# Kernel optimization log

Hardware: AMD Instinct MI355X
Metric: run time of the kernel (lower is better)

## Reference

```python
import jax, jax.numpy as jnp
import numpy as np

B, S, DM, H, DK, DH = 8, 1024, 512, 8, 32, 64
LN_EPS = 1e-5
NEG_SLOPE = 0.01  # torch LeakyReLU default


def _l2norm(t, axis=-1, eps=1e-12):
    # matches F.normalize(p=2): x / max(||x||, eps)
    n = jnp.sqrt(jnp.sum(t * t, axis=axis, keepdims=True))
    return t / jnp.maximum(n, eps)


def _layernorm(t, w, b, eps=LN_EPS):
    mu = jnp.mean(t, axis=-1, keepdims=True)
    var = jnp.mean((t - mu) ** 2, axis=-1, keepdims=True)
    return (t - mu) * jax.lax.rsqrt(var + eps) * w + b


def setup_inputs() -> dict:
    key = jax.random.key(0)
    ks = jax.random.split(key, 16)
    x = jax.random.normal(ks[0], (B, S, DM), dtype=jnp.float32)
    # causal-style mask: True = masked (upper triangle)
    attn_mask = jnp.broadcast_to(jnp.triu(jnp.ones((S, S), dtype=bool), k=1), (B, S, S))
    pairwise_dist = jax.random.uniform(ks[1], (B, S, S), dtype=jnp.float32)
    s = 0.02
    return {
        "x": x,
        "attn_mask": attn_mask,
        "pairwise_dist": pairwise_dist,
        "Wq": jax.random.normal(ks[2], (H, DK, DM), dtype=jnp.float32) * s,
        "Wk": jax.random.normal(ks[3], (H, DK, DM), dtype=jnp.float32) * s,
        "Wv": jax.random.normal(ks[4], (H, DH, DM), dtype=jnp.float32) * s,
        "omega": jnp.ones((H,), dtype=jnp.float32),
        "Wo": jax.random.normal(ks[5], (DM, H * DH), dtype=jnp.float32) * s,
        "bo": jnp.zeros((DM,), dtype=jnp.float32),
        "Wf": jax.random.normal(ks[6], (DM, DM), dtype=jnp.float32) * s,
        "bf": jnp.zeros((DM,), dtype=jnp.float32),
        "ln1_w": jnp.ones((DM,), dtype=jnp.float32),
        "ln1_b": jnp.zeros((DM,), dtype=jnp.float32),
        "ln2_w": jnp.ones((DM,), dtype=jnp.float32),
        "ln2_b": jnp.zeros((DM,), dtype=jnp.float32),
    }


def _encoder_layer(x, attn_mask, pairwise_dist, Wq, Wk, Wv, omega,
                   Wo, bo, Wf, bf, ln1_w, ln1_b, ln2_w, ln2_b):
    # --- multi-head self-attention, all heads batched ---
    q = _l2norm(jnp.einsum('bsd,hkd->hbsk', x, Wq))   # [H,B,S,DK]
    k = _l2norm(jnp.einsum('bsd,hkd->hbsk', x, Wk))
    v = jnp.einsum('bsd,hvd->hbsv', x, Wv)            # [H,B,S,DH]
    scores = jnp.einsum('hbsk,hbtk->hbst', q, k)      # cosine-sim, [H,B,S,S]
    # distance bias: exp(-omega*d) - 1, detached in the original
    r = jax.lax.stop_gradient(
        jnp.exp(-omega[:, None, None, None] * pairwise_dist[None]) - 1.0)
    scores = scores + r
    scores = jnp.where(attn_mask[None], -jnp.inf, scores)
    # custom softmax: exp(x) / (sum + 1); exp(-inf)=0 handles masking
    z = jnp.exp(scores)
    attn = z / (jnp.sum(z, axis=-1, keepdims=True) + 1.0)
    y = jnp.einsum('hbst,hbtv->hbsv', attn, v)        # [H,B,S,DH]
    y = jnp.transpose(y, (1, 2, 0, 3)).reshape(x.shape[0], x.shape[1], -1)  # concat heads
    x_attn = y @ Wo.T + bo
    # --- residual + LN + FFN (dropout p=0 -> identity) ---
    z1 = _layernorm(x + x_attn, ln1_w, ln1_b)
    z_ff = jax.nn.leaky_relu(z1 @ Wf.T + bf, negative_slope=NEG_SLOPE)
    return _layernorm(z1 + z_ff, ln2_w, ln2_b)


def reference(x, attn_mask, pairwise_dist, Wq, Wk, Wv, omega,
              Wo, bo, Wf, bf, ln1_w, ln1_b, ln2_w, ln2_b):
    return _encoder_layer(x, attn_mask, pairwise_dist, Wq, Wk, Wv, omega,
                          Wo, bo, Wf, bf, ln1_w, ln1_b, ln2_w, ln2_b)
```

## Files before the change

### kernel.cpp

```cpp
#include <hip/hip_runtime.h>
#include <hip/hip_bf16.h>
#include <math.h>
#include <stdint.h>

#define BB 8
#define SS 1024
#define DMM 512
#define HH 8
#define DKK 32
#define DHH 64

typedef __bf16 bf16x8 __attribute__((ext_vector_type(8)));
typedef float f32x4 __attribute__((ext_vector_type(4)));

__device__ __forceinline__ void gll16(const void* g, void* l) {
  __builtin_amdgcn_global_load_lds(
      (const __attribute__((address_space(1))) void*)(uintptr_t)g,
      (__attribute__((address_space(3))) void*)(uint32_t)(uintptr_t)l,
      16, 0, 0);
}

__device__ __forceinline__ uint4 pack8(const float4 a, const float4 b) {
  union { __hip_bfloat162 h2[4]; uint4 u; } p;
  p.h2[0] = __float22bfloat162_rn(make_float2(a.x, a.y));
  p.h2[1] = __float22bfloat162_rn(make_float2(a.z, a.w));
  p.h2[2] = __float22bfloat162_rn(make_float2(b.x, b.y));
  p.h2[3] = __float22bfloat162_rn(make_float2(b.z, b.w));
  return p.u;
}

__global__ __launch_bounds__(256) void cvt_all(
    const float* __restrict__ x, const float* __restrict__ Wq,
    const float* __restrict__ Wk, const float* __restrict__ Wv,
    const float* __restrict__ Wo, const float* __restrict__ Wf,
    __bf16* __restrict__ xb, __bf16* __restrict__ Wcat,
    __bf16* __restrict__ Wob, __bf16* __restrict__ Wfb) {
  size_t i = ((size_t)blockIdx.x * 256 + threadIdx.x) * 8;
  const float* s;
  __bf16* d;
  size_t off;
  if (i < 4194304) { s = x; d = xb + i; off = i; }
  else {
    size_t j = i - 4194304;
    if (j < 524288) {
      d = Wcat + j;
      if (j < 131072) { s = Wq; off = j; }
      else if (j < 262144) { s = Wk; off = j - 131072; }
      else { s = Wv; off = j - 262144; }
    } else {
      size_t jj = j - 524288;
      if (jj < 262144) { s = Wo; d = Wob + jj; off = jj; }
      else { s = Wf; d = Wfb + (jj - 262144); off = jj - 262144; }
    }
  }
  float4 a = *(const float4*)&s[off];
  float4 b = *(const float4*)&s[off + 4];
  *(uint4*)d = pack8(a, b);
}

__global__ __launch_bounds__(256) void gemm_qkv(
    const __bf16* __restrict__ A, const __bf16* __restrict__ W,
    __bf16* __restrict__ Qg, __bf16* __restrict__ Kg,
    __bf16* __restrict__ Vrow) {
  __shared__ __bf16 As[128 * 32];
  __shared__ __bf16 Bs[128 * 32];
  const int tid = threadIdx.x;
  const int n0 = blockIdx.x * 128;
  const int m0 = blockIdx.y * 128;
  const int lane = tid & 63;
  const int w = tid >> 6;
  const int wm = (w & 1) * 64, wn = (w >> 1) * 64;
  const int fr = lane & 15, quad = lane >> 4;
  const int srow = lane >> 2;
  const int schunk = (lane & 3) ^ ((lane >> 3) & 3);

  f32x4 acc[4][4];
#pragma unroll
  for (int mi = 0; mi < 4; ++mi)
#pragma unroll
    for (int ni = 0; ni < 4; ++ni) acc[mi][ni] = (f32x4){0.f, 0.f, 0.f, 0.f};

  for (int kt = 0; kt < 512; kt += 32) {
    __syncthreads();
#pragma unroll
    for (int j = 0; j < 2; ++j) {
      const int seg = w * 2 + j;
      const int row = seg * 16 + srow;
      gll16(&A[(size_t)(m0 + row) * 512 + kt + schunk * 8], &As[seg * 512]);
      gll16(&W[(size_t)(n0 + row) * 512 + kt + schunk * 8], &Bs[seg * 512]);
    }
    __syncthreads();

    bf16x8 af[4], bf[4];
    const int rsw = (quad ^ ((fr >> 1) & 3)) * 8;
#pragma unroll
    for (int mi = 0; mi < 4; ++mi)
      af[mi] = *(const bf16x8*)&As[(wm + mi * 16 + fr) * 32 + rsw];
#pragma unroll
    for (int ni = 0; ni < 4; ++ni)
      bf[ni] = *(const bf16x8*)&Bs[(wn + ni * 16 + fr) * 32 + rsw];
#pragma unroll
    for (int mi = 0; mi < 4; ++mi)
#pragma unroll
      for (int ni = 0; ni < 4; ++ni)
        acc[mi][ni] = __builtin_amdgcn_mfma_f32_16x16x32_bf16(
            af[mi], bf[ni], acc[mi][ni], 0, 0, 0);
  }

  const int er = quad * 4;
  const int ec = fr;
  if (n0 < 512) {
    const bool isq = (n0 < 256);
    __bf16* G = isq ? Qg : Kg;
    const int nb = isq ? n0 : n0 - 256;
#pragma unroll
    for (int mi = 0; mi < 4; ++mi) {
#pragma unroll
      for (int p = 0; p < 2; ++p) {
        const int hh = (nb + wn + p * 32) >> 5;
#pragma unroll
        for (int r = 0; r < 4; ++r) {
          float v0 = acc[mi][2 * p][r], v1 = acc[mi][2 * p + 1][r];
          float ss = v0 * v0 + v1 * v1;
          ss += __shfl_xor(ss, 1, 64);
          ss += __shfl_xor(ss, 2, 64);
          ss += __shfl_xor(ss, 4, 64);
          ss += __shfl_xor(ss, 8, 64);
          const float sc = 1.0f / fmaxf(sqrtf(ss), 1e-12f);
          const int mm = m0 + wm + mi * 16 + er + r;
          const int bb = mm >> 10, s = mm & 1023;
          __bf16* gp = G + ((size_t)(bb * 8 + hh) * 1024 + s) * 32;
          gp[ec] = (__bf16)(v0 * sc);
          gp[16 + ec] = (__bf16)(v1 * sc);
        }
      }
    }
  } else {
#pragma unroll
    for (int mi = 0; mi < 4; ++mi)
#pragma unroll
      for (int ni = 0; ni < 4; ++ni) {
        const int n = n0 - 512 + wn + ni * 16 + ec;
#pragma unroll
        for (int r = 0; r < 4; ++r) {
          const int mm = m0 + wm + mi * 16 + er + r;
          Vrow[(size_t)mm * 512 + n] = (__bf16)acc[mi][ni][r];
        }
      }
  }
}

template <int MODE>
__global__ __launch_bounds__(256) void gemm_bf16(
    const __bf16* __restrict__ A, const __bf16* __restrict__ W,
    const float* __restrict__ bias, const float* __restrict__ resid,
    float* __restrict__ C, int N) {
  __shared__ __bf16 As[128 * 32];
  __shared__ __bf16 Bs[128 * 32];
  const int tid = threadIdx.x;
  const int n0 = blockIdx.x * 128;
  const int m0 = blockIdx.y * 128;
  const int lane = tid & 63;
  const int w = tid >> 6;
  const int wm = (w & 1) * 64, wn = (w >> 1) * 64;
  const int fr = lane & 15, quad = lane >> 4;
  const int srow = lane >> 2;
  const int schunk = (lane & 3) ^ ((lane >> 3) & 3);

  f32x4 acc[4][4];
#pragma unroll
  for (int mi = 0; mi < 4; ++mi)
#pragma unroll
    for (int ni = 0; ni < 4; ++ni) acc[mi][ni] = (f32x4){0.f, 0.f, 0.f, 0.f};

  for (int kt = 0; kt < 512; kt += 32) {
    __syncthreads();
#pragma unroll
    for (int j = 0; j < 2; ++j) {
      const int seg = w * 2 + j;
      const int row = seg * 16 + srow;
      gll16(&A[(size_t)(m0 + row) * 512 + kt + schunk * 8], &As[seg * 512]);
      gll16(&W[(size_t)(n0 + row) * 512 + kt + schunk * 8], &Bs[seg * 512]);
    }
    __syncthreads();

    bf16x8 af[4], bf[4];
    const int rsw = (quad ^ ((fr >> 1) & 3)) * 8;
#pragma unroll
    for (int mi = 0; mi < 4; ++mi)
      af[mi] = *(const bf16x8*)&As[(wm + mi * 16 + fr) * 32 + rsw];
#pragma unroll
    for (int ni = 0; ni < 4; ++ni)
      bf[ni] = *(const bf16x8*)&Bs[(wn + ni * 16 + fr) * 32 + rsw];
#pragma unroll
    for (int mi = 0; mi < 4; ++mi)
#pragma unroll
      for (int ni = 0; ni < 4; ++ni)
        acc[mi][ni] = __builtin_amdgcn_mfma_f32_16x16x32_bf16(
            af[mi], bf[ni], acc[mi][ni], 0, 0, 0);
  }

  const int er = quad * 4;
  const int ec = fr;
#pragma unroll
  for (int mi = 0; mi < 4; ++mi) {
#pragma unroll
    for (int ni = 0; ni < 4; ++ni) {
      const int n = n0 + wn + ni * 16 + ec;
      float bsv = bias[n];
#pragma unroll
      for (int r = 0; r < 4; ++r) {
        const int m = m0 + wm + mi * 16 + er + r;
        float v = acc[mi][ni][r];
        if (MODE == 1) {
          v += bsv + resid[(size_t)m * 512 + n];
        } else {
          float g = v + bsv;
          g = g > 0.f ? g : 0.01f * g;
          v = resid[(size_t)m * 512 + n] + g;
        }
        C[(size_t)m * N + n] = v;
      }
    }
  }
}

__global__ __launch_bounds__(256) void v_transpose(
    const __bf16* __restrict__ Vrow, __bf16* __restrict__ Vt) {
  __shared__ __bf16 vt[64][136];
  const int bh = blockIdx.x;
  const int b = bh >> 3, h = bh & 7;
  const int sb = blockIdx.y * 128;
  const int tid = threadIdx.x;
#pragma unroll
  for (int i = 0; i < 8; ++i) {
    int idx = tid + i * 256;
    int t = idx >> 4, vd4 = (idx & 15) * 4;
    union { uint2 u; __bf16 e[4]; } v;
    v.u = *(const uint2*)&Vrow[((size_t)(b * 1024 + sb + t)) * 512 + h * 64 + vd4];
    vt[vd4 + 0][t] = v.e[0];
    vt[vd4 + 1][t] = v.e[1];
    vt[vd4 + 2][t] = v.e[2];
    vt[vd4 + 3][t] = v.e[3];
  }
  __syncthreads();
  {
    const int vd = tid >> 2, tseg = (tid & 3) * 32;
    uint4* o = (uint4*)(Vt + (size_t)bh * 65536 + (size_t)vd * 1024 + sb + tseg);
#pragma unroll
    for (int j = 0; j < 4; ++j)
      o[j] = *(const uint4*)&vt[vd][tseg + j * 8];
  }
}

__global__ __launch_bounds__(256) void attn_fused(
    const __bf16* __restrict__ Qg, const __bf16* __restrict__ Kg,
    const __bf16* __restrict__ Vt, const float* __restrict__ dist,
    const float* __restrict__ omega, __bf16* __restrict__ y) {
  __shared__ __bf16 Ks[64 * 32];
  __shared__ __bf16 Vs[64 * 64];
  __shared__ __bf16 zbuf[4][16][72];

  const int b = blockIdx.x;
  const int s0 = (15 - blockIdx.y) * 64;
  const int h = blockIdx.z;
  const int bh = b * 8 + h;
  const int tid = threadIdx.x;
  const int lane = tid & 63;
  const int w = tid >> 6;
  const int q = lane >> 4;
  const int m = lane & 15;
  const float om = omega[h];

  const int sl = s0 + w * 16 + m;
  const bf16x8 bq = *(const bf16x8*)&Qg[((size_t)bh * 1024 + sl) * 32 + q * 8];
  const int kswz = (q ^ ((m >> 1) & 3)) * 8;

  f32x4 acc[4];
#pragma unroll
  for (int ni = 0; ni < 4; ++ni) acc[ni] = (f32x4){0.f, 0.f, 0.f, 0.f};
  float zsum = 0.0f;
  const int ntiles = (s0 >> 6) + 1;

  for (int tt = 0; tt < ntiles; ++tt) {
    const int t0 = tt * 64;
    __syncthreads();
    {
      int row = tid >> 2, p = tid & 3;
      uint4 v = *(const uint4*)&Kg[((size_t)bh * 1024 + t0 + row) * 32 + p * 8];
      *(uint4*)&Ks[row * 32 + ((p ^ ((row >> 1) & 3)) * 8)] = v;
    }
#pragma unroll
    for (int i = 0; i < 2; ++i) {
      int idx = tid + i * 256;
      int vd = idx >> 3, p = idx & 7;
      uint4 v = *(const uint4*)&Vt[(size_t)bh * 65536 + (size_t)vd * 1024 + t0 + p * 8];
      *(uint4*)&Vs[vd * 64 + ((p ^ (vd & 7)) * 8)] = v;
    }
    float4 dv[4];
#pragma unroll
    for (int mi = 0; mi < 4; ++mi)
      dv[mi] = *(const float4*)&dist[((size_t)b * 1024 + sl) * 1024 + t0 + 16 * mi + q * 4];
    __syncthreads();

#pragma unroll
    for (int mi = 0; mi < 4; ++mi) {
      const bf16x8 ak = *(const bf16x8*)&Ks[(16 * mi + m) * 32 + kswz];
      f32x4 s4 = __builtin_amdgcn_mfma_f32_16x16x32_bf16(
          ak, bq, (f32x4){0.f, 0.f, 0.f, 0.f}, 0, 0, 0);
      float zr[4];
#pragma unroll
      for (int r = 0; r < 4; ++r) {
        const int t = t0 + 16 * mi + q * 4 + r;
        float zv = __expf(s4[r] + __expf(-om * (&dv[mi].x)[r]) - 1.0f);
        zr[r] = (t <= sl) ? zv : 0.0f;
        zsum += zr[r];
      }
      union { __hip_bfloat162 h2[2]; uint2 u; } pz;
      pz.h2[0] = __float22bfloat162_rn(make_float2(zr[0], zr[1]));
      pz.h2[1] = __float22bfloat162_rn(make_float2(zr[2], zr[3]));
      *(uint2*)&zbuf[w][m][16 * mi + q * 4] = pz.u;
    }
    const bf16x8 az0 = *(const bf16x8*)&zbuf[w][m][q * 8];
    const bf16x8 az1 = *(const bf16x8*)&zbuf[w][m][32 + q * 8];
#pragma unroll
    for (int ni = 0; ni < 4; ++ni) {
      const bf16x8 vb0 = *(const bf16x8*)&Vs[(16 * ni + m) * 64 + ((q ^ (m & 7)) * 8)];
      const bf16x8 vb1 = *(const bf16x8*)&Vs[(16 * ni + m) * 64 + (((q + 4) ^ (m & 7)) * 8)];
      acc[ni] = __builtin_amdgcn_mfma_f32_16x16x32_bf16(az0, vb0, acc[ni], 0, 0, 0);
      acc[ni] = __builtin_amdgcn_mfma_f32_16x16x32_bf16(az1, vb1, acc[ni], 0, 0, 0);
    }
  }

  zsum += __shfl_xor(zsum, 16, 64);
  zsum += __shfl_xor(zsum, 32, 64);

#pragma unroll
  for (int r = 0; r < 4; ++r) {
    const float dn = __shfl(zsum, q * 4 + r, 64);
    const float inv = 1.0f / (dn + 1.0f);
    __bf16* yp = &y[((size_t)b * 1024 + s0 + w * 16 + q * 4 + r) * 512 + h * 64 + m];
#pragma unroll
    for (int ni = 0; ni < 4; ++ni)
      yp[ni * 16] = (__bf16)(acc[ni][r] * inv);
  }
}

__global__ __launch_bounds__(256) void ln_kernel(
    const float* __restrict__ in, const float* __restrict__ w,
    const float* __restrict__ bvec, float* __restrict__ out,
    __bf16* __restrict__ outb) {
  const int row = blockIdx.x * 4 + (threadIdx.x >> 6);
  const int lane = threadIdx.x & 63;
  const float4* ip = (const float4*)(in + (size_t)row * 512);
  float4 a = ip[lane * 2], c = ip[lane * 2 + 1];
  float s = a.x + a.y + a.z + a.w + c.x + c.y + c.z + c.w;
#pragma unroll
  for (int off = 32; off > 0; off >>= 1) s += __shfl_xor(s, off, 64);
  const float mu = s * (1.0f / 512.0f);
  a.x -= mu; a.y -= mu; a.z -= mu; a.w -= mu;
  c.x -= mu; c.y -= mu; c.z -= mu; c.w -= mu;
  float s2 = a.x * a.x + a.y * a.y + a.z * a.z + a.w * a.w +
             c.x * c.x + c.y * c.y + c.z * c.z + c.w * c.w;
#pragma unroll
  for (int off = 32; off > 0; off >>= 1) s2 += __shfl_xor(s2, off, 64);
  const float inv = rsqrtf(s2 * (1.0f / 512.0f) + 1e-5f);
  const float4 w0 = ((const float4*)w)[lane * 2], w1 = ((const float4*)w)[lane * 2 + 1];
  const float4 b0 = ((const float4*)bvec)[lane * 2], b1 = ((const float4*)bvec)[lane * 2 + 1];
  float4 o0, o1;
  o0.x = a.x * inv * w0.x + b0.x; o0.y = a.y * inv * w0.y + b0.y;
  o0.z = a.z * inv * w0.z + b0.z; o0.w = a.w * inv * w0.w + b0.w;
  o1.x = c.x * inv * w1.x + b1.x; o1.y = c.y * inv * w1.y + b1.y;
  o1.z = c.z * inv * w1.z + b1.z; o1.w = c.w * inv * w1.w + b1.w;
  float4* op = (float4*)(out + (size_t)row * 512);
  op[lane * 2] = o0; op[lane * 2 + 1] = o1;
  if (outb) *(uint4*)&outb[(size_t)row * 512 + lane * 8] = pack8(o0, o1);
}

extern "C" void kernel_launch(void* const* d_in, const int* in_sizes, int n_in,
                              void* d_out, int out_size, void* d_ws, size_t ws_size,
                              hipStream_t stream) {
  const float* x = (const float*)d_in[0];
  const float* dist = (const float*)d_in[2];
  const float* Wq = (const float*)d_in[3];
  const float* Wk = (const float*)d_in[4];
  const float* Wv = (const float*)d_in[5];
  const float* omega = (const float*)d_in[6];
  const float* Wo = (const float*)d_in[7];
  const float* bo = (const float*)d_in[8];
  const float* Wf = (const float*)d_in[9];
  const float* bf_ = (const float*)d_in[10];
  const float* ln1w = (const float*)d_in[11];
  const float* ln1b = (const float*)d_in[12];
  const float* ln2w = (const float*)d_in[13];
  const float* ln2b = (const float*)d_in[14];
  float* out = (float*)d_out;

  char* base = (char*)d_ws;
  const size_t MB = 1 << 20;
  __bf16* xb = (__bf16*)base;
  __bf16* yb = (__bf16*)base;
  __bf16* Wcat = (__bf16*)(base + 8 * MB);
  __bf16* Wob = (__bf16*)(base + 9 * MB);
  __bf16* Wfb = (__bf16*)(base + 9 * MB + 512 * 1024);
  __bf16* Qg = (__bf16*)(base + 10 * MB);
  __bf16* Kg = (__bf16*)(base + 14 * MB);
  __bf16* Vrow = (__bf16*)(base + 18 * MB);
  __bf16* Vt = (__bf16*)(base + 26 * MB);
  float* t1 = (float*)(base + 18 * MB);
  __bf16* t1b = (__bf16*)(base + 34 * MB);

  dim3 blk(256);
  cvt_all<<<dim3(2560), blk, 0, stream>>>(x, Wq, Wk, Wv, Wo, Wf,
                                          xb, Wcat, Wob, Wfb);
  gemm_qkv<<<dim3(8, 64), blk, 0, stream>>>(xb, Wcat, Qg, Kg, Vrow);
  v_transpose<<<dim3(64, 8), blk, 0, stream>>>(Vrow, Vt);
  attn_fused<<<dim3(8, 16, 8), blk, 0, stream>>>(Qg, Kg, Vt, dist, omega, yb);
  gemm_bf16<1><<<dim3(4, 64), blk, 0, stream>>>(yb, Wob, bo, x, t1, 512);
  ln_kernel<<<dim3(2048), blk, 0, stream>>>(t1, ln1w, ln1b, t1, t1b);
  gemm_bf16<2><<<dim3(4, 64), blk, 0, stream>>>(t1b, Wfb, bf_, t1, out, 512);
  ln_kernel<<<dim3(2048), blk, 0, stream>>>(out, ln2w, ln2b, out, nullptr);
}
```

Before: 246.3 us.

## Split long causal attention rows across blocks and double-buffer GEMM LDS tiles

The causal attention grid is rebalanced with constant tables. Query blocks 8-15 are split into two key-range halves that write fp32 partial accumulators and row sums, and a new reduce kernel combines them and normalizes. This evens out per-block work so the longest blocks no longer dominate the tail, at the cost of extra global traffic and one more launch. Separately, both GEMM kernels now double-buffer their LDS tiles, issuing the next tile's loads before computing on the current one, which removes one barrier per k-step.

```diff
diff --git a/kernel.cpp b/kernel.cpp
--- a/kernel.cpp
+++ b/kernel.cpp
@@ -28,6 +28,10 @@
   p.h2[3] = __float22bfloat162_rn(make_float2(b.z, b.w));
   return p.u;
 }
+
+__device__ __constant__ unsigned char dJ[24]  = {15,15,14,7,14,13,13,12,6,12,11,11,10,5,10,9,9,8,4,8,3,2,1,0};
+__device__ __constant__ unsigned char dTB[24] = {0,8,0,0,8,0,7,0,0,7,0,6,0,0,6,0,5,0,0,5,0,0,0,0};
+__device__ __constant__ unsigned char dTE[24] = {8,16,8,8,15,7,14,7,7,13,6,12,6,6,11,5,10,5,5,9,4,3,2,1};
 
 __global__ __launch_bounds__(256) void cvt_all(
     const float* __restrict__ x, const float* __restrict__ Wq,
@@ -62,8 +66,8 @@
     const __bf16* __restrict__ A, const __bf16* __restrict__ W,
     __bf16* __restrict__ Qg, __bf16* __restrict__ Kg,
     __bf16* __restrict__ Vrow) {
-  __shared__ __bf16 As[128 * 32];
-  __shared__ __bf16 Bs[128 * 32];
+  __shared__ __bf16 As[2][128 * 32];
+  __shared__ __bf16 Bs[2][128 * 32];
   const int tid = threadIdx.x;
   const int n0 = blockIdx.x * 128;
   const int m0 = blockIdx.y * 128;
@@ -80,31 +84,41 @@
 #pragma unroll
     for (int ni = 0; ni < 4; ++ni) acc[mi][ni] = (f32x4){0.f, 0.f, 0.f, 0.f};
 
-  for (int kt = 0; kt < 512; kt += 32) {
+#pragma unroll
+  for (int j = 0; j < 2; ++j) {
+    const int seg = w * 2 + j;
+    const int row = seg * 16 + srow;
+    gll16(&A[(size_t)(m0 + row) * 512 + schunk * 8], &As[0][seg * 512]);
+    gll16(&W[(size_t)(n0 + row) * 512 + schunk * 8], &Bs[0][seg * 512]);
+  }
+  for (int it = 0; it < 16; ++it) {
     __syncthreads();
-#pragma unroll
-    for (int j = 0; j < 2; ++j) {
-      const int seg = w * 2 + j;
-      const int row = seg * 16 + srow;
-      gll16(&A[(size_t)(m0 + row) * 512 + kt + schunk * 8], &As[seg * 512]);
-      gll16(&W[(size_t)(n0 + row) * 512 + kt + schunk * 8], &Bs[seg * 512]);
-    }
-    __syncthreads();
-
-    bf16x8 af[4], bf[4];
+    if (it < 15) {
+      const int kt = (it + 1) * 32, ib = (it + 1) & 1;
+#pragma unroll
+      for (int j = 0; j < 2; ++j) {
+        const int seg = w * 2 + j;
+        const int row = seg * 16 + srow;
+        gll16(&A[(size_t)(m0 + row) * 512 + kt + schunk * 8], &As[ib][seg * 512]);
+        gll16(&W[(size_t)(n0 + row) * 512 + kt + schunk * 8], &Bs[ib][seg * 512]);
+      }
+    }
+    const __bf16* as = As[it & 1];
+    const __bf16* bs = Bs[it & 1];
+    bf16x8 af[4], bfv[4];
     const int rsw = (quad ^ ((fr >> 1) & 3)) * 8;
 #pragma unroll
     for (int mi = 0; mi < 4; ++mi)
-      af[mi] = *(const bf16x8*)&As[(wm + mi * 16 + fr) * 32 + rsw];
+      af[mi] = *(const bf16x8*)&as[(wm + mi * 16 + fr) * 32 + rsw];
 #pragma unroll
     for (int ni = 0; ni < 4; ++ni)
-      bf[ni] = *(const bf16x8*)&Bs[(wn + ni * 16 + fr) * 32 + rsw];
+      bfv[ni] = *(const bf16x8*)&bs[(wn + ni * 16 + fr) * 32 + rsw];
 #pragma unroll
     for (int mi = 0; mi < 4; ++mi)
 #pragma unroll
       for (int ni = 0; ni < 4; ++ni)
         acc[mi][ni] = __builtin_amdgcn_mfma_f32_16x16x32_bf16(
-            af[mi], bf[ni], acc[mi][ni], 0, 0, 0);
+            af[mi], bfv[ni], acc[mi][ni], 0, 0, 0);
   }
 
   const int er = quad * 4;
@@ -155,8 +169,8 @@
     const __bf16* __restrict__ A, const __bf16* __restrict__ W,
     const float* __restrict__ bias, const float* __restrict__ resid,
     float* __restrict__ C, int N) {
-  __shared__ __bf16 As[128 * 32];
-  __shared__ __bf16 Bs[128 * 32];
+  __shared__ __bf16 As[2][128 * 32];
+  __shared__ __bf16 Bs[2][128 * 32];
   const int tid = threadIdx.x;
   const int n0 = blockIdx.x * 128;
   const int m0 = blockIdx.y * 128;
@@ -173,31 +187,41 @@
 #pragma unroll
     for (int ni = 0; ni < 4; ++ni) acc[mi][ni] = (f32x4){0.f, 0.f, 0.f, 0.f};
 
-  for (int kt = 0; kt < 512; kt += 32) {
+#pragma unroll
+  for (int j = 0; j < 2; ++j) {
+    const int seg = w * 2 + j;
+    const int row = seg * 16 + srow;
+    gll16(&A[(size_t)(m0 + row) * 512 + schunk * 8], &As[0][seg * 512]);
+    gll16(&W[(size_t)(n0 + row) * 512 + schunk * 8], &Bs[0][seg * 512]);
+  }
+  for (int it = 0; it < 16; ++it) {
     __syncthreads();
-#pragma unroll
-    for (int j = 0; j < 2; ++j) {
-      const int seg = w * 2 + j;
-      const int row = seg * 16 + srow;
-      gll16(&A[(size_t)(m0 + row) * 512 + kt + schunk * 8], &As[seg * 512]);
-      gll16(&W[(size_t)(n0 + row) * 512 + kt + schunk * 8], &Bs[seg * 512]);
-    }
-    __syncthreads();
-
-    bf16x8 af[4], bf[4];
+    if (it < 15) {
+      const int kt = (it + 1) * 32, ib = (it + 1) & 1;
+#pragma unroll
+      for (int j = 0; j < 2; ++j) {
+        const int seg = w * 2 + j;
+        const int row = seg * 16 + srow;
+        gll16(&A[(size_t)(m0 + row) * 512 + kt + schunk * 8], &As[ib][seg * 512]);
+        gll16(&W[(size_t)(n0 + row) * 512 + kt + schunk * 8], &Bs[ib][seg * 512]);
+      }
+    }
+    const __bf16* as = As[it & 1];
+    const __bf16* bs = Bs[it & 1];
+    bf16x8 af[4], bfv[4];
     const int rsw = (quad ^ ((fr >> 1) & 3)) * 8;
 #pragma unroll
     for (int mi = 0; mi < 4; ++mi)
-      af[mi] = *(const bf16x8*)&As[(wm + mi * 16 + fr) * 32 + rsw];
+      af[mi] = *(const bf16x8*)&as[(wm + mi * 16 + fr) * 32 + rsw];
 #pragma unroll
     for (int ni = 0; ni < 4; ++ni)
-      bf[ni] = *(const bf16x8*)&Bs[(wn + ni * 16 + fr) * 32 + rsw];
+      bfv[ni] = *(const bf16x8*)&bs[(wn + ni * 16 + fr) * 32 + rsw];
 #pragma unroll
     for (int mi = 0; mi < 4; ++mi)
 #pragma unroll
       for (int ni = 0; ni < 4; ++ni)
         acc[mi][ni] = __builtin_amdgcn_mfma_f32_16x16x32_bf16(
-            af[mi], bf[ni], acc[mi][ni], 0, 0, 0);
+            af[mi], bfv[ni], acc[mi][ni], 0, 0, 0);
   }
 
   const int er = quad * 4;
@@ -256,15 +280,19 @@
 __global__ __launch_bounds__(256) void attn_fused(
     const __bf16* __restrict__ Qg, const __bf16* __restrict__ Kg,
     const __bf16* __restrict__ Vt, const float* __restrict__ dist,
-    const float* __restrict__ omega, __bf16* __restrict__ y) {
+    const float* __restrict__ omega, __bf16* __restrict__ y,
+    float* __restrict__ Pacc, float* __restrict__ Zb) {
   __shared__ __bf16 Ks[64 * 32];
   __shared__ __bf16 Vs[64 * 64];
   __shared__ __bf16 zbuf[4][16][72];
 
-  const int b = blockIdx.x;
-  const int s0 = (15 - blockIdx.y) * 64;
-  const int h = blockIdx.z;
-  const int bh = b * 8 + h;
+  const int bh = blockIdx.x;
+  const int entry = blockIdx.y;
+  const int b = bh >> 3, h = bh & 7;
+  const int jidx = dJ[entry];
+  const int tbeg = dTB[entry];
+  const int tend = dTE[entry];
+  const int s0 = jidx * 64;
   const int tid = threadIdx.x;
   const int lane = tid & 63;
   const int w = tid >> 6;
@@ -280,9 +308,8 @@
 #pragma unroll
   for (int ni = 0; ni < 4; ++ni) acc[ni] = (f32x4){0.f, 0.f, 0.f, 0.f};
   float zsum = 0.0f;
-  const int ntiles = (s0 >> 6) + 1;
-
-  for (int tt = 0; tt < ntiles; ++tt) {
+
+  for (int tt = tbeg; tt < tend; ++tt) {
     const int t0 = tt * 64;
     __syncthreads();
     {
@@ -335,15 +362,56 @@
   zsum += __shfl_xor(zsum, 16, 64);
   zsum += __shfl_xor(zsum, 32, 64);
 
-#pragma unroll
-  for (int r = 0; r < 4; ++r) {
-    const float dn = __shfl(zsum, q * 4 + r, 64);
-    const float inv = 1.0f / (dn + 1.0f);
-    __bf16* yp = &y[((size_t)b * 1024 + s0 + w * 16 + q * 4 + r) * 512 + h * 64 + m];
-#pragma unroll
-    for (int ni = 0; ni < 4; ++ni)
-      yp[ni * 16] = (__bf16)(acc[ni][r] * inv);
-  }
+  if (jidx < 8) {
+#pragma unroll
+    for (int r = 0; r < 4; ++r) {
+      const float dn = __shfl(zsum, q * 4 + r, 64);
+      const float inv = 1.0f / (dn + 1.0f);
+      __bf16* yp = &y[((size_t)b * 1024 + s0 + w * 16 + q * 4 + r) * 512 + h * 64 + m];
+#pragma unroll
+      for (int ni = 0; ni < 4; ++ni)
+        yp[ni * 16] = (__bf16)(acc[ni][r] * inv);
+    }
+  } else {
+    const int half = (tbeg != 0) ? 1 : 0;
+    const size_t pidx = (size_t)((bh * 8 + (jidx - 8)) * 2 + half);
+    float* Pp = Pacc + pidx * 4096;
+    float* Zp = Zb + pidx * 64;
+#pragma unroll
+    for (int r = 0; r < 4; ++r) {
+      const int row = w * 16 + q * 4 + r;
+      const float dn = __shfl(zsum, q * 4 + r, 64);
+      if (m == 0) Zp[row] = dn;
+#pragma unroll
+      for (int ni = 0; ni < 4; ++ni)
+        Pp[row * 64 + ni * 16 + m] = acc[ni][r];
+    }
+  }
+}
+
+__global__ __launch_bounds__(256) void attn_reduce(
+    const float* __restrict__ Pacc, const float* __restrict__ Zb,
+    __bf16* __restrict__ y) {
+  const int e = blockIdx.x;
+  const int bh = e >> 3, j = (e & 7) + 8;
+  const int b = bh >> 3, h = bh & 7;
+  const float* p0 = Pacc + (size_t)e * 2 * 4096;
+  const float* p1 = p0 + 4096;
+  const int row = threadIdx.x >> 2;
+  const int c0 = (threadIdx.x & 3) * 16;
+  const float z = Zb[(size_t)e * 128 + row] + Zb[(size_t)e * 128 + 64 + row];
+  const float inv = 1.0f / (z + 1.0f);
+  float4 o[4];
+#pragma unroll
+  for (int i = 0; i < 4; ++i) {
+    const float4 a = *(const float4*)&p0[row * 64 + c0 + i * 4];
+    const float4 c = *(const float4*)&p1[row * 64 + c0 + i * 4];
+    o[i].x = (a.x + c.x) * inv; o[i].y = (a.y + c.y) * inv;
+    o[i].z = (a.z + c.z) * inv; o[i].w = (a.w + c.w) * inv;
+  }
+  __bf16* yp = &y[((size_t)b * 1024 + j * 64 + row) * 512 + h * 64 + c0];
+  *(uint4*)yp = pack8(o[0], o[1]);
+  *(uint4*)(yp + 8) = pack8(o[2], o[3]);
 }
 
 __global__ __launch_bounds__(256) void ln_kernel(
@@ -406,16 +474,20 @@
   __bf16* Qg = (__bf16*)(base + 10 * MB);
   __bf16* Kg = (__bf16*)(base + 14 * MB);
   __bf16* Vrow = (__bf16*)(base + 18 * MB);
-  __bf16* Vt = (__bf16*)(base + 26 * MB);
+  float* Pacc = (float*)(base + 18 * MB);
   float* t1 = (float*)(base + 18 * MB);
+  __bf16* Vt = (__bf16*)(base + 34 * MB);
   __bf16* t1b = (__bf16*)(base + 34 * MB);
+  float* Zb = (float*)(base + 42 * MB);
 
   dim3 blk(256);
   cvt_all<<<dim3(2560), blk, 0, stream>>>(x, Wq, Wk, Wv, Wo, Wf,
                                           xb, Wcat, Wob, Wfb);
   gemm_qkv<<<dim3(8, 64), blk, 0, stream>>>(xb, Wcat, Qg, Kg, Vrow);
   v_transpose<<<dim3(64, 8), blk, 0, stream>>>(Vrow, Vt);
-  attn_fused<<<dim3(8, 16, 8), blk, 0, stream>>>(Qg, Kg, Vt, dist, omega, yb);
+  attn_fused<<<dim3(64, 24), blk, 0, stream>>>(Qg, Kg, Vt, dist, omega, yb,
+                                               Pacc, Zb);
+  attn_reduce<<<dim3(512), blk, 0, stream>>>(Pacc, Zb, yb);
   gemm_bf16<1><<<dim3(4, 64), blk, 0, stream>>>(yb, Wob, bo, x, t1, 512);
   ln_kernel<<<dim3(2048), blk, 0, stream>>>(t1, ln1w, ln1b, t1, t1b);
   gemm_bf16<2><<<dim3(4, 64), blk, 0, stream>>>(t1b, Wfb, bf_, t1, out, 512);
```

New measurement: 261.4 us. 1.06x slower.
